# Optimization experiments

Hardware: AMD Instinct MI355X
Metric: run time of the kernel (lower is better)

The kernel has to match this reference:

```python
import jax, jax.numpy as jnp
import numpy as np


def setup_inputs() -> dict:
    key = jax.random.key(0)
    k1, k2, k3 = jax.random.split(key, 3)
    shape = (32, 64, 128, 128)  # B, C, H, W
    out = jax.random.normal(k1, shape, dtype=jnp.float32)
    vals = jax.random.normal(k2, shape, dtype=jnp.float32)
    keep = jax.random.uniform(k3, shape) < 0.1
    target = jnp.where(keep, vals, 0.0).astype(jnp.float32)
    return {"out": out, "target": target}


def reference(out, target):
    # Original loops over every nonzero index of target and sums
    # F.smooth_l1_loss (beta=1, mean over a single scalar == elementwise value).
    # Equivalent fused form: masked elementwise smooth-L1, summed.
    d = jnp.abs(out - target)
    sl1 = jnp.where(d < 1.0, 0.5 * d * d, d - 0.5)
    mask = target != 0.0
    return jnp.sum(jnp.where(mask, sl1, 0.0))
```

## Files before the change

### kernel.cpp

```cpp
#include <hip/hip_runtime.h>


typedef float v4f __attribute__((ext_vector_type(4)));

#define BLOCK 1024
#define ITERS 4
#define CHUNK (BLOCK * ITERS)
#define NWAVES (BLOCK / 64)

__device__ __forceinline__ float sl1_masked(float o, float t) {
    float d = fabsf(o - t);
    float s = (d < 1.0f) ? (0.5f * d * d) : (d - 0.5f);
    return (t != 0.0f) ? s : 0.0f;
}

__device__ __forceinline__ float sl1_v4(v4f o, v4f t) {
    return sl1_masked(o.x, t.x) + sl1_masked(o.y, t.y) +
           sl1_masked(o.z, t.z) + sl1_masked(o.w, t.w);
}

__global__ __launch_bounds__(BLOCK) void sl1_partial_kernel(
    const v4f* __restrict__ o4,
    const v4f* __restrict__ t4,
    float* __restrict__ partials,
    long long n4)
{
    const long long base = (long long)blockIdx.x * CHUNK + threadIdx.x;
    float acc = 0.0f;

    if (base + (ITERS - 1) * BLOCK < n4) {
        v4f o[ITERS], t[ITERS];
        #pragma unroll
        for (int k = 0; k < ITERS; ++k) {
            o[k] = o4[base + k * BLOCK];
            t[k] = t4[base + k * BLOCK];
        }
        #pragma unroll
        for (int k = 0; k < ITERS; ++k)
            acc += sl1_v4(o[k], t[k]);
    } else {
        #pragma unroll
        for (int k = 0; k < ITERS; ++k) {
            long long idx = base + (long long)k * BLOCK;
            if (idx < n4) {
                v4f o = o4[idx];
                v4f t = t4[idx];
                acc += sl1_v4(o, t);
            }
        }
    }

    #pragma unroll
    for (int off = 32; off > 0; off >>= 1)
        acc += __shfl_down(acc, off, 64);
    __shared__ float wave_sums[NWAVES];
    const int lane = threadIdx.x & 63;
    const int wave = threadIdx.x >> 6;
    if (lane == 0) wave_sums[wave] = acc;
    __syncthreads();
    if (threadIdx.x == 0) {
        float s = 0.0f;
        #pragma unroll
        for (int w = 0; w < NWAVES; ++w) s += wave_sums[w];
        partials[blockIdx.x] = s;
    }
}

__global__ __launch_bounds__(256) void sl1_final_kernel(
    const float* __restrict__ partials,
    float* __restrict__ result,
    int n)
{
    float acc = 0.0f;
    for (int i = threadIdx.x; i < n; i += 256)
        acc += partials[i];
    #pragma unroll
    for (int off = 32; off > 0; off >>= 1)
        acc += __shfl_down(acc, off, 64);
    __shared__ float wave_sums[4];
    const int lane = threadIdx.x & 63;
    const int wave = threadIdx.x >> 6;
    if (lane == 0) wave_sums[wave] = acc;
    __syncthreads();
    if (threadIdx.x == 0)
        result[0] = wave_sums[0] + wave_sums[1] + wave_sums[2] + wave_sums[3];
}

extern "C" void kernel_launch(void* const* d_in, const int* in_sizes, int n_in,
                              void* d_out, int out_size, void* d_ws, size_t ws_size,
                              hipStream_t stream) {
    const v4f* o4 = (const v4f*)d_in[0];
    const v4f* t4 = (const v4f*)d_in[1];
    float* res      = (float*)d_out;
    float* partials = (float*)d_ws;

    const long long n  = (long long)in_sizes[0];
    const long long n4 = n / 4;

    const int grid = (int)((n4 + CHUNK - 1) / CHUNK);
    sl1_partial_kernel<<<grid, BLOCK, 0, stream>>>(o4, t4, partials, n4);
    sl1_final_kernel<<<1, 256, 0, stream>>>(partials, res, grid);
}
```

Baseline: 273.8 us.

## Replace vectorized one-shot blocks with scalar grid-stride loop over fixed grid

Replaces the float4-vectorized kernel, where each block handled a fixed chunk with all loads issued up front, with a scalar grid-stride loop over a fixed 512-block grid. This cuts the number of partial sums and the size of the final reduction, and removes the tail-handling branch. In exchange it drops the 128-bit vector loads and the explicit memory-level parallelism per thread. It also narrows indices to 32-bit, which limits the supported input size.

```diff
diff --git a/kernel.cpp b/kernel.cpp
--- a/kernel.cpp
+++ b/kernel.cpp
@@ -1,53 +1,24 @@
 #include <hip/hip_runtime.h>
 
 
-typedef float v4f __attribute__((ext_vector_type(4)));
-
 #define BLOCK 1024
-#define ITERS 4
-#define CHUNK (BLOCK * ITERS)
+#define GRID  512
 #define NWAVES (BLOCK / 64)
 
-__device__ __forceinline__ float sl1_masked(float o, float t) {
-    float d = fabsf(o - t);
-    float s = (d < 1.0f) ? (0.5f * d * d) : (d - 0.5f);
-    return (t != 0.0f) ? s : 0.0f;
-}
-
-__device__ __forceinline__ float sl1_v4(v4f o, v4f t) {
-    return sl1_masked(o.x, t.x) + sl1_masked(o.y, t.y) +
-           sl1_masked(o.z, t.z) + sl1_masked(o.w, t.w);
-}
-
 __global__ __launch_bounds__(BLOCK) void sl1_partial_kernel(
-    const v4f* __restrict__ o4,
-    const v4f* __restrict__ t4,
+    const float* __restrict__ o,
+    const float* __restrict__ t,
     float* __restrict__ partials,
-    long long n4)
+    int n)
 {
-    const long long base = (long long)blockIdx.x * CHUNK + threadIdx.x;
+    const int stride = GRID * BLOCK;
     float acc = 0.0f;
-
-    if (base + (ITERS - 1) * BLOCK < n4) {
-        v4f o[ITERS], t[ITERS];
-        #pragma unroll
-        for (int k = 0; k < ITERS; ++k) {
-            o[k] = o4[base + k * BLOCK];
-            t[k] = t4[base + k * BLOCK];
-        }
-        #pragma unroll
-        for (int k = 0; k < ITERS; ++k)
-            acc += sl1_v4(o[k], t[k]);
-    } else {
-        #pragma unroll
-        for (int k = 0; k < ITERS; ++k) {
-            long long idx = base + (long long)k * BLOCK;
-            if (idx < n4) {
-                v4f o = o4[idx];
-                v4f t = t4[idx];
-                acc += sl1_v4(o, t);
-            }
-        }
+    for (int i = blockIdx.x * BLOCK + threadIdx.x; i < n; i += stride) {
+        float ov = o[i];
+        float tv = t[i];
+        float d  = fabsf(ov - tv);
+        float s  = (d < 1.0f) ? (0.5f * d * d) : (d - 0.5f);
+        acc     += (tv != 0.0f) ? s : 0.0f;
     }
 
     #pragma unroll
@@ -89,15 +60,13 @@
 extern "C" void kernel_launch(void* const* d_in, const int* in_sizes, int n_in,
                               void* d_out, int out_size, void* d_ws, size_t ws_size,
                               hipStream_t stream) {
-    const v4f* o4 = (const v4f*)d_in[0];
-    const v4f* t4 = (const v4f*)d_in[1];
+    const float* o = (const float*)d_in[0];
+    const float* t = (const float*)d_in[1];
     float* res      = (float*)d_out;
     float* partials = (float*)d_ws;
 
-    const long long n  = (long long)in_sizes[0];
-    const long long n4 = n / 4;
+    const int n = in_sizes[0];
 
-    const int grid = (int)((n4 + CHUNK - 1) / CHUNK);
-    sl1_partial_kernel<<<grid, BLOCK, 0, stream>>>(o4, t4, partials, n4);
-    sl1_final_kernel<<<1, 256, 0, stream>>>(partials, res, grid);
+    sl1_partial_kernel<<<GRID, BLOCK, 0, stream>>>(o, t, partials, n);
+    sl1_final_kernel<<<1, 256, 0, stream>>>(partials, res, GRID);
 }
```

After: 273.5 us. No clear change (-0.1%).
